# Kernel optimization log

Measured on AMD Instinct MI355X. Metric: run time of the kernel, lower is better.

Reference implementation:

```python
import jax, jax.numpy as jnp
import numpy as np

B, N = 8, 1024
C = [256, 512, 1024]
C2 = C[1]
KV = sum(C)            # 1792
H = 4                  # num_attention_heads
EXPAND = 4
LN_EPS = 1e-6
IN_EPS = 1e-5          # nn.InstanceNorm2d default eps


def setup_inputs() -> dict:
    key = jax.random.key(0)
    ks = jax.random.split(key, 16)
    s = 0.02
    inp = {
        "emb1": jax.random.normal(ks[0], (B, N, C[0]), jnp.float32),
        "emb2": jax.random.normal(ks[1], (B, N, C[1]), jnp.float32),
        "emb3": jax.random.normal(ks[2], (B, N, C[2]), jnp.float32),
        # per-head projection weights stored as [in, out] (torch Linear applies x @ W.T)
        "Wq": jax.random.normal(ks[3], (H, C2, C2), jnp.float32) * s,
        "Wk": jax.random.normal(ks[4], (H, KV, KV), jnp.float32) * s,
        "Wv": jax.random.normal(ks[5], (H, KV, KV), jnp.float32) * s,
        "Wout": jax.random.normal(ks[6], (C2, C2), jnp.float32) * s,
        "ln1_g": jnp.ones((C2,), jnp.float32),
        "ln1_b": jnp.zeros((C2,), jnp.float32),
        "lnall_g": jnp.ones((KV,), jnp.float32),
        "lnall_b": jnp.zeros((KV,), jnp.float32),
        "lnffn_g": jnp.ones((C2,), jnp.float32),
        "lnffn_b": jnp.zeros((C2,), jnp.float32),
        "fc1_w": jax.random.normal(ks[7], (C2, C2 * EXPAND), jnp.float32) * s,
        "fc1_b": jnp.zeros((C2 * EXPAND,), jnp.float32),
        "fc2_w": jax.random.normal(ks[8], (C2 * EXPAND, C2), jnp.float32) * s,
        "fc2_b": jnp.zeros((C2,), jnp.float32),
    }
    return inp


def _layer_norm(x, g, b, eps=LN_EPS):
    m = jnp.mean(x, axis=-1, keepdims=True)
    v = jnp.var(x, axis=-1, keepdims=True)
    return (x - m) * jax.lax.rsqrt(v + eps) * g + b


def _instance_norm2d(x, eps=IN_EPS):
    # x: [B, H, C2, KV]; normalize each (B,H) map over its last two dims (no affine)
    m = jnp.mean(x, axis=(-2, -1), keepdims=True)
    v = jnp.var(x, axis=(-2, -1), keepdims=True)
    return (x - m) * jax.lax.rsqrt(v + eps)


def reference(emb1, emb2, emb3, Wq, Wk, Wv, Wout,
              ln1_g, ln1_b, lnall_g, lnall_b, lnffn_g, lnffn_b,
              fc1_w, fc1_b, fc2_w, fc2_b):
    org2 = emb2
    emb_all = jnp.concatenate([emb1, emb2, emb3], axis=2)        # [B,N,KV]
    cx2 = _layer_norm(emb2, ln1_g, ln1_b)                         # [B,N,C2]
    emb_all = _layer_norm(emb_all, lnall_g, lnall_b)              # [B,N,KV]

    # batched per-head projections (replaces the Python ModuleList loop)
    q = jnp.einsum('bnc,hcd->bhnd', cx2, Wq)                      # [B,H,N,C2]
    k = jnp.einsum('bnc,hcd->bhnd', emb_all, Wk)                  # [B,H,N,KV]
    v = jnp.einsum('bnc,hcd->bhnd', emb_all, Wv)                  # [B,H,N,KV]

    # channel attention: q^T k over the token axis
    scores = jnp.einsum('bhnc,bhnk->bhck', q, k) / np.sqrt(KV)    # [B,H,C2,KV]
    probs = jax.nn.softmax(_instance_norm2d(scores), axis=3)      # [B,H,C2,KV]

    # context = probs @ v^T, then mean over heads (fused into one einsum)
    ctx = jnp.einsum('bhck,bhnk->bnc', probs, v) / H              # [B,N,C2]
    o = ctx @ Wout                                                # [B,N,C2]

    cx2 = org2 + o
    x2 = _layer_norm(cx2, lnffn_g, lnffn_b)
    x2 = jax.nn.gelu(x2 @ fc1_w + fc1_b, approximate=False)
    x2 = x2 @ fc2_w + fc2_b
    return x2 + cx2
```

## Files before the change

kernel.cpp:

```cpp
#include <hip/hip_runtime.h>
#include <cstdint>
#include <cmath>

typedef __bf16 bf16_t;
typedef __attribute__((ext_vector_type(8))) __bf16 bf16x8;
typedef __attribute__((ext_vector_type(4))) float f32x4;

#define AS_G(x) ((__attribute__((address_space(1))) void*)(x))
#define AS_L(x) ((__attribute__((address_space(3))) void*)(x))

#define BK 64

#define BSZ 8
#define NTOK 1024
#define CC2 512
#define KVD 1792
#define NH 4
#define FFD 2048
#define ROWS 8192


__device__ __forceinline__ void stage_pair(const bf16_t* __restrict__ A,
                                           const bf16_t* __restrict__ B,
                                           int ld, bf16_t* ldsA, bf16_t* ldsB, int tid)
{
#pragma unroll
  for (int it = 0; it < 4; ++it) {
    int chunk = it * 256 + tid;
    int r = chunk >> 3;
    int s = chunk & 7;
    int cg = ((s ^ (r & 7)) << 3);
    __builtin_amdgcn_global_load_lds(AS_G(A + (long)r * ld + cg),
                                     AS_L(ldsA + chunk * 8), 16, 0, 0);
    __builtin_amdgcn_global_load_lds(AS_G(B + (long)r * ld + cg),
                                     AS_L(ldsB + chunk * 8), 16, 0, 0);
  }
}

__device__ __forceinline__ void mfma_step(const bf16_t* ldsA, const bf16_t* ldsB,
                                          f32x4 acc[4][4], int wr, int wc, int lane, int kc)
{
  const int quad = lane >> 4, l16 = lane & 15;
  bf16x8 a[4], b[4];
#pragma unroll
  for (int i = 0; i < 4; ++i) {
    int r = wr * 64 + i * 16 + l16;
    int slot = (kc + quad) ^ (r & 7);
    a[i] = *(const bf16x8*)(ldsA + r * BK + slot * 8);
  }
#pragma unroll
  for (int j = 0; j < 4; ++j) {
    int r = wc * 64 + j * 16 + l16;
    int slot = (kc + quad) ^ (r & 7);
    b[j] = *(const bf16x8*)(ldsB + r * BK + slot * 8);
  }
#pragma unroll
  for (int i = 0; i < 4; ++i)
#pragma unroll
    for (int j = 0; j < 4; ++j)
      acc[i][j] = __builtin_amdgcn_mfma_f32_16x16x32_bf16(a[i], b[j], acc[i][j], 0, 0, 0);
}

#define GEMM_PROLOG() \
  __shared__ __align__(16) bf16_t ldsA[128 * BK]; \
  __shared__ __align__(16) bf16_t ldsB[128 * BK]; \
  const int tid = threadIdx.x; \
  const int wave = tid >> 6, lane = tid & 63; \
  const int wr = wave >> 1, wc = wave & 1; \
  f32x4 acc[4][4] = {};

#define GEMM_LOOP(Aptr, Bptr, Kdim) \
  for (int k0 = 0; k0 < (Kdim); k0 += BK) { \
    stage_pair((Aptr) + k0, (Bptr) + k0, (Kdim), ldsA, ldsB, tid); \
    __syncthreads(); \
    mfma_step(ldsA, ldsB, acc, wr, wc, lane, 0); \
    mfma_step(ldsA, ldsB, acc, wr, wc, lane, 4); \
    __syncthreads(); \
  }

template <typename F>
__device__ __forceinline__ void epilogue_apply(f32x4 acc[4][4], int wr, int wc, int lane, F f)
{
  const int quad = lane >> 4, l16 = lane & 15;
#pragma unroll
  for (int i = 0; i < 4; ++i)
#pragma unroll
    for (int j = 0; j < 4; ++j)
#pragma unroll
      for (int r = 0; r < 4; ++r)
        f(wr * 64 + i * 16 + quad * 4 + r, wc * 64 + j * 16 + l16, acc[i][j][r]);
}


__global__ void zstats_k(float* s)
{
  if (threadIdx.x < 64) s[threadIdx.x] = 0.f;
}

__global__ __launch_bounds__(256) void tconv_k(const float* __restrict__ in,
                                               bf16_t* __restrict__ out, int R, int Cc)
{
  __shared__ float tile[32][33];
  const long base = (long)blockIdx.z * R * Cc;
  const int c0 = blockIdx.x * 32, r0 = blockIdx.y * 32;
  const int tx = threadIdx.x & 31, ty = threadIdx.x >> 5;
#pragma unroll
  for (int i = 0; i < 4; ++i)
    tile[ty + i * 8][tx] = in[base + (long)(r0 + ty + i * 8) * Cc + c0 + tx];
  __syncthreads();
#pragma unroll
  for (int i = 0; i < 4; ++i)
    out[base + (long)(c0 + ty + i * 8) * R + r0 + tx] = (bf16_t)tile[tx][ty + i * 8];
}

__global__ __launch_bounds__(256) void tconv_bf_k(const bf16_t* __restrict__ in,
                                                  bf16_t* __restrict__ out, int R, int Cc)
{
  __shared__ float tile[32][33];
  const long base = (long)blockIdx.z * R * Cc;
  const int c0 = blockIdx.x * 32, r0 = blockIdx.y * 32;
  const int tx = threadIdx.x & 31, ty = threadIdx.x >> 5;
#pragma unroll
  for (int i = 0; i < 4; ++i)
    tile[ty + i * 8][tx] = (float)in[base + (long)(r0 + ty + i * 8) * Cc + c0 + tx];
  __syncthreads();
#pragma unroll
  for (int i = 0; i < 4; ++i)
    out[base + (long)(c0 + ty + i * 8) * R + r0 + tx] = (bf16_t)tile[tx][ty + i * 8];
}

__global__ __launch_bounds__(256) void cast_k(const float* __restrict__ in,
                                              bf16_t* __restrict__ out, long n)
{
  long i = ((long)blockIdx.x * 256 + threadIdx.x) * 4;
  if (i + 3 < n) {
    float4 v = *(const float4*)(in + i);
    out[i] = (bf16_t)v.x; out[i + 1] = (bf16_t)v.y;
    out[i + 2] = (bf16_t)v.z; out[i + 3] = (bf16_t)v.w;
  }
}

__global__ __launch_bounds__(256) void ln_concat_k(const float* __restrict__ e1,
                                                   const float* __restrict__ e2,
                                                   const float* __restrict__ e3,
                                                   const float* __restrict__ g1,
                                                   const float* __restrict__ b1,
                                                   const float* __restrict__ ga,
                                                   const float* __restrict__ ba,
                                                   bf16_t* __restrict__ cxln,
                                                   bf16_t* __restrict__ embln)
{
  const long row = blockIdx.x;
  const float* p1 = e1 + row * 256;
  const float* p2 = e2 + row * 512;
  const float* p3 = e3 + row * 1024;
  const int t = threadIdx.x;
  float vals[7];
  float sa = 0.f, qa = 0.f;
#pragma unroll
  for (int i = 0; i < 7; ++i) {
    int idx = t + i * 256;
    float x = (idx < 256) ? p1[idx] : (idx < 768 ? p2[idx - 256] : p3[idx - 768]);
    vals[i] = x;
    sa += x; qa += x * x;
  }
  float s2 = vals[1] + vals[2];
  float q2 = vals[1] * vals[1] + vals[2] * vals[2];
  for (int off = 32; off; off >>= 1) {
    sa += __shfl_down(sa, off, 64); qa += __shfl_down(qa, off, 64);
    s2 += __shfl_down(s2, off, 64); q2 += __shfl_down(q2, off, 64);
  }
  __shared__ float red[4][4];
  const int wave = t >> 6, lane = t & 63;
  if (lane == 0) { red[0][wave] = sa; red[1][wave] = qa; red[2][wave] = s2; red[3][wave] = q2; }
  __syncthreads();
  float SA = red[0][0] + red[0][1] + red[0][2] + red[0][3];
  float QA = red[1][0] + red[1][1] + red[1][2] + red[1][3];
  float S2 = red[2][0] + red[2][1] + red[2][2] + red[2][3];
  float Q2 = red[3][0] + red[3][1] + red[3][2] + red[3][3];
  float ma = SA * (1.f / 1792.f);
  float va = QA * (1.f / 1792.f) - ma * ma;
  float rsa = rsqrtf(va + 1e-6f);
  float m2 = S2 * (1.f / 512.f);
  float v2 = Q2 * (1.f / 512.f) - m2 * m2;
  float rs2 = rsqrtf(v2 + 1e-6f);
#pragma unroll
  for (int i = 0; i < 7; ++i) {
    int idx = t + i * 256;
    embln[row * 1792 + idx] = (bf16_t)((vals[i] - ma) * rsa * ga[idx] + ba[idx]);
  }
  cxln[row * 512 + t]       = (bf16_t)((vals[1] - m2) * rs2 * g1[t] + b1[t]);
  cxln[row * 512 + t + 256] = (bf16_t)((vals[2] - m2) * rs2 * g1[t + 256] + b1[t + 256]);
}

__global__ __launch_bounds__(256) void ln2_k(const float* __restrict__ X,
                                             const float* __restrict__ g,
                                             const float* __restrict__ bb,
                                             bf16_t* __restrict__ Y)
{
  const long row = blockIdx.x;
  const float* p = X + row * 512;
  const int t = threadIdx.x;
  float x0 = p[t], x1 = p[t + 256];
  float s = x0 + x1, q = x0 * x0 + x1 * x1;
  for (int off = 32; off; off >>= 1) {
    s += __shfl_down(s, off, 64); q += __shfl_down(q, off, 64);
  }
  __shared__ float red[2][4];
  const int wave = t >> 6, lane = t & 63;
  if (lane == 0) { red[0][wave] = s; red[1][wave] = q; }
  __syncthreads();
  float S = red[0][0] + red[0][1] + red[0][2] + red[0][3];
  float Q = red[1][0] + red[1][1] + red[1][2] + red[1][3];
  float m = S * (1.f / 512.f);
  float v = Q * (1.f / 512.f) - m * m;
  float rs = rsqrtf(v + 1e-6f);
  Y[row * 512 + t]       = (bf16_t)((x0 - m) * rs * g[t] + bb[t]);
  Y[row * 512 + t + 256] = (bf16_t)((x1 - m) * rs * g[t + 256] + bb[t + 256]);
}

__global__ __launch_bounds__(256) void softmax_k(bf16_t* __restrict__ SC,
                                                 const float* __restrict__ stats)
{
  const long rowid = blockIdx.x;
  const int z = (int)(rowid >> 9);
  const float inv_cnt = 1.f / (512.f * 1792.f);
  float m = stats[2 * z] * inv_cnt;
  float var = stats[2 * z + 1] * inv_cnt - m * m;
  float rs = rsqrtf(var + 1e-5f);
  bf16_t* rowp = SC + rowid * 1792;
  const int t = threadIdx.x;
  float v[7];
  float mx = -1e30f;
#pragma unroll
  for (int i = 0; i < 7; ++i) {
    v[i] = (float)rowp[t + i * 256] * rs;
    mx = fmaxf(mx, v[i]);
  }
  for (int off = 32; off; off >>= 1) mx = fmaxf(mx, __shfl_down(mx, off, 64));
  __shared__ float red[8];
  const int wave = t >> 6, lane = t & 63;
  if (lane == 0) red[wave] = mx;
  __syncthreads();
  mx = fmaxf(fmaxf(red[0], red[1]), fmaxf(red[2], red[3]));
  float sum = 0.f;
#pragma unroll
  for (int i = 0; i < 7; ++i) { v[i] = __expf(v[i] - mx); sum += v[i]; }
  for (int off = 32; off; off >>= 1) sum += __shfl_down(sum, off, 64);
  if (lane == 0) red[4 + wave] = sum;
  __syncthreads();
  float inv = 1.f / (red[4] + red[5] + red[6] + red[7]);
#pragma unroll
  for (int i = 0; i < 7; ++i) rowp[t + i * 256] = (bf16_t)(v[i] * inv);
}


__global__ __launch_bounds__(256) void gemm_ab(const bf16_t* __restrict__ A, long astride,
                                               const bf16_t* __restrict__ B, long bstride,
                                               bf16_t* __restrict__ C, long cstride,
                                               int K, int ldc)
{
  const int z = blockIdx.z;
  GEMM_PROLOG();
  const bf16_t* Ap = A + z * astride + (long)blockIdx.x * 128 * K;
  const bf16_t* Bp = B + z * bstride + (long)blockIdx.y * 128 * K;
  GEMM_LOOP(Ap, Bp, K);
  bf16_t* Cb = C + (long)z * cstride;
  const int rbase = blockIdx.x * 128, cbase = blockIdx.y * 128;
  epilogue_apply(acc, wr, wc, lane, [&](int rr, int cc, float v) {
    Cb[(long)(rbase + rr) * ldc + cbase + cc] = (bf16_t)v;
  });
}

__global__ __launch_bounds__(256) void gemm_t1(const bf16_t* __restrict__ WqT,
                                               const bf16_t* __restrict__ Gt,
                                               bf16_t* __restrict__ T1)
{
  const int z = blockIdx.z, hh = z >> 3, b = z & 7;
  GEMM_PROLOG();
  const bf16_t* Ap = WqT + (long)hh * CC2 * CC2 + (long)blockIdx.x * 128 * CC2;
  const bf16_t* Bp = Gt + (long)b * KVD * CC2 + (long)blockIdx.y * 128 * CC2;
  GEMM_LOOP(Ap, Bp, CC2);
  bf16_t* Cb = T1 + (long)z * CC2 * KVD;
  const int rbase = blockIdx.x * 128, cbase = blockIdx.y * 128;
  epilogue_apply(acc, wr, wc, lane, [&](int rr, int cc, float v) {
    Cb[(long)(rbase + rr) * KVD + cbase + cc] = (bf16_t)v;
  });
}

__global__ __launch_bounds__(256) void gemm_scores(const bf16_t* __restrict__ T1,
                                                   const bf16_t* __restrict__ WkT,
                                                   bf16_t* __restrict__ SC,
                                                   float* __restrict__ stats)
{
  const int z = blockIdx.z, hh = z >> 3;
  GEMM_PROLOG();
  const bf16_t* Ap = T1 + (long)z * CC2 * KVD + (long)blockIdx.x * 128 * KVD;
  const bf16_t* Bp = WkT + (long)hh * KVD * KVD + (long)blockIdx.y * 128 * KVD;
  GEMM_LOOP(Ap, Bp, KVD);
  const float scale = 0.02362277854f;
  bf16_t* Cb = SC + (long)z * CC2 * KVD;
  const int rbase = blockIdx.x * 128, cbase = blockIdx.y * 128;
  float s = 0.f, q = 0.f;
  epilogue_apply(acc, wr, wc, lane, [&](int rr, int cc, float v) {
    v *= scale;
    Cb[(long)(rbase + rr) * KVD + cbase + cc] = (bf16_t)v;
    s += v; q += v * v;
  });
  for (int off = 32; off; off >>= 1) { s += __shfl_down(s, off, 64); q += __shfl_down(q, off, 64); }
  __shared__ float red[8];
  if (lane == 0) { red[wave] = s; red[4 + wave] = q; }
  __syncthreads();
  if (tid == 0) {
    atomicAdd(&stats[2 * z],     red[0] + red[1] + red[2] + red[3]);
    atomicAdd(&stats[2 * z + 1], red[4] + red[5] + red[6] + red[7]);
  }
}

__global__ __launch_bounds__(256) void gemm_macc(const bf16_t* __restrict__ P,
                                                 const bf16_t* __restrict__ WvB,
                                                 bf16_t* __restrict__ M, int first)
{
  const int z = blockIdx.z, hh = z >> 3;
  GEMM_PROLOG();
  const bf16_t* Ap = P + (long)z * CC2 * KVD + (long)blockIdx.x * 128 * KVD;
  const bf16_t* Bp = WvB + (long)hh * KVD * KVD + (long)blockIdx.y * 128 * KVD;
  GEMM_LOOP(Ap, Bp, KVD);
  bf16_t* Cb = M + (long)z * CC2 * KVD;
  const int rbase = blockIdx.x * 128, cbase = blockIdx.y * 128;
  epilogue_apply(acc, wr, wc, lane, [&](int rr, int cc, float v) {
    long idx = (long)(rbase + rr) * KVD + cbase + cc;
    float prev = first ? 0.f : (float)Cb[idx];
    Cb[idx] = (bf16_t)(prev + v * 0.25f);
  });
}

__global__ __launch_bounds__(256) void gemm_ctx(const bf16_t* __restrict__ E,
                                                const bf16_t* __restrict__ Msum,
                                                bf16_t* __restrict__ CTX)
{
  const int b = blockIdx.z;
  GEMM_PROLOG();
  const bf16_t* Ap = E + (long)b * NTOK * KVD + (long)blockIdx.x * 128 * KVD;
  const bf16_t* Bp0 = Msum + (long)b * CC2 * KVD + (long)blockIdx.y * 128 * KVD;
  const bf16_t* Bp1 = Msum + (long)(8 + b) * CC2 * KVD + (long)blockIdx.y * 128 * KVD;
  GEMM_LOOP(Ap, Bp0, KVD);
  GEMM_LOOP(Ap, Bp1, KVD);
  bf16_t* Cb = CTX + (long)b * NTOK * CC2;
  const int rbase = blockIdx.x * 128, cbase = blockIdx.y * 128;
  epilogue_apply(acc, wr, wc, lane, [&](int rr, int cc, float v) {
    Cb[(long)(rbase + rr) * CC2 + cbase + cc] = (bf16_t)v;
  });
}

__global__ __launch_bounds__(256) void gemm_resid(const bf16_t* __restrict__ A,
                                                  const bf16_t* __restrict__ B,
                                                  const float* __restrict__ emb2,
                                                  float* __restrict__ CX2)
{
  GEMM_PROLOG();
  const bf16_t* Ap = A + (long)blockIdx.x * 128 * CC2;
  const bf16_t* Bp = B + (long)blockIdx.y * 128 * CC2;
  GEMM_LOOP(Ap, Bp, CC2);
  const int rbase = blockIdx.x * 128, cbase = blockIdx.y * 128;
  epilogue_apply(acc, wr, wc, lane, [&](int rr, int cc, float v) {
    long idx = (long)(rbase + rr) * CC2 + cbase + cc;
    CX2[idx] = v + emb2[idx];
  });
}

__global__ __launch_bounds__(256) void gemm_gelu(const bf16_t* __restrict__ A,
                                                 const bf16_t* __restrict__ B,
                                                 const float* __restrict__ bias,
                                                 bf16_t* __restrict__ H)
{
  GEMM_PROLOG();
  const bf16_t* Ap = A + (long)blockIdx.x * 128 * CC2;
  const bf16_t* Bp = B + (long)blockIdx.y * 128 * CC2;
  GEMM_LOOP(Ap, Bp, CC2);
  const int rbase = blockIdx.x * 128, cbase = blockIdx.y * 128;
  epilogue_apply(acc, wr, wc, lane, [&](int rr, int cc, float v) {
    float x = v + bias[cbase + cc];
    float g = 0.5f * x * (1.0f + erff(x * 0.70710678118f));
    H[(long)(rbase + rr) * FFD + cbase + cc] = (bf16_t)g;
  });
}

__global__ __launch_bounds__(256) void gemm_out(const bf16_t* __restrict__ A,
                                                const bf16_t* __restrict__ B,
                                                const float* __restrict__ bias,
                                                const float* __restrict__ CX2,
                                                float* __restrict__ OUT)
{
  GEMM_PROLOG();
  const bf16_t* Ap = A + (long)blockIdx.x * 128 * FFD;
  const bf16_t* Bp = B + (long)blockIdx.y * 128 * FFD;
  GEMM_LOOP(Ap, Bp, FFD);
  const int rbase = blockIdx.x * 128, cbase = blockIdx.y * 128;
  epilogue_apply(acc, wr, wc, lane, [&](int rr, int cc, float v) {
    long idx = (long)(rbase + rr) * CC2 + cbase + cc;
    OUT[idx] = v + bias[cbase + cc] + CX2[idx];
  });
}


extern "C" void kernel_launch(void* const* d_in, const int* in_sizes, int n_in,
                              void* d_out, int out_size, void* d_ws, size_t ws_size,
                              hipStream_t stream)
{
  const float* emb1   = (const float*)d_in[0];
  const float* emb2   = (const float*)d_in[1];
  const float* emb3   = (const float*)d_in[2];
  const float* Wq     = (const float*)d_in[3];
  const float* Wk     = (const float*)d_in[4];
  const float* Wv     = (const float*)d_in[5];
  const float* Wout   = (const float*)d_in[6];
  const float* ln1_g  = (const float*)d_in[7];
  const float* ln1_b  = (const float*)d_in[8];
  const float* lnall_g = (const float*)d_in[9];
  const float* lnall_b = (const float*)d_in[10];
  const float* lnffn_g = (const float*)d_in[11];
  const float* lnffn_b = (const float*)d_in[12];
  const float* fc1_w  = (const float*)d_in[13];
  const float* fc1_b  = (const float*)d_in[14];
  const float* fc2_w  = (const float*)d_in[15];
  const float* fc2_b  = (const float*)d_in[16];
  float* out = (float*)d_out;

  char* ws = (char*)d_ws;
  size_t off = 0;
  auto alloc = [&](size_t bytes) {
    size_t r = off;
    off = (off + bytes + 255) & ~(size_t)255;
    return r;
  };

  size_t oEMBLN = alloc((size_t)ROWS * KVD * 2);
  size_t oCXLN  = alloc((size_t)ROWS * CC2 * 2);
  size_t oCX2   = alloc((size_t)ROWS * CC2 * 4);
  size_t oGt    = alloc((size_t)BSZ * KVD * CC2 * 2);
  size_t oMsum  = alloc((size_t)16 * CC2 * KVD * 2);
  size_t oWOT   = alloc((size_t)CC2 * CC2 * 2);
  size_t oF1T   = alloc((size_t)FFD * CC2 * 2);
  size_t oF2T   = alloc((size_t)CC2 * FFD * 2);
  size_t oSTATS = alloc(64 * 4);
  size_t oSCR   = alloc(0);
  size_t oCXLNT  = alloc((size_t)BSZ * CC2 * NTOK * 2);
  size_t oEMBLNT = alloc((size_t)BSZ * KVD * NTOK * 2);
  (void)ws_size; (void)in_sizes; (void)n_in; (void)out_size;

  bf16_t* EMBLN  = (bf16_t*)(ws + oEMBLN);
  bf16_t* CXLN   = (bf16_t*)(ws + oCXLN);
  float*  CX2    = (float*)(ws + oCX2);
  bf16_t* Gt     = (bf16_t*)(ws + oGt);
  bf16_t* Msum   = (bf16_t*)(ws + oMsum);
  bf16_t* WOT    = (bf16_t*)(ws + oWOT);
  bf16_t* F1T    = (bf16_t*)(ws + oF1T);
  bf16_t* F2T    = (bf16_t*)(ws + oF2T);
  float*  STATS  = (float*)(ws + oSTATS);
  bf16_t* CXLNT  = (bf16_t*)(ws + oCXLNT);
  bf16_t* EMBLNT = (bf16_t*)(ws + oEMBLNT);
  char* scr = ws + oSCR;
  auto rnd = [](size_t v) { return (v + 255) & ~(size_t)255; };
  bf16_t* WqT = (bf16_t*)(scr);
  bf16_t* WkT = (bf16_t*)(scr + rnd((size_t)2 * CC2 * CC2 * 2));
  bf16_t* WvB = (bf16_t*)((char*)WkT + rnd((size_t)2 * KVD * KVD * 2));
  bf16_t* T1  = (bf16_t*)((char*)WvB + rnd((size_t)2 * KVD * KVD * 2));
  bf16_t* SC  = (bf16_t*)((char*)T1 + rnd((size_t)16 * CC2 * KVD * 2));
  bf16_t* CTX  = (bf16_t*)(scr);
  bf16_t* FFNH = (bf16_t*)(scr + rnd((size_t)ROWS * CC2 * 2));
  bf16_t* X2LN = CXLN;

  zstats_k<<<1, 64, 0, stream>>>(STATS);
  tconv_k<<<dim3(16, 16), 256, 0, stream>>>(Wout, WOT, 512, 512);
  tconv_k<<<dim3(64, 16), 256, 0, stream>>>(fc1_w, F1T, 512, 2048);
  tconv_k<<<dim3(16, 64), 256, 0, stream>>>(fc2_w, F2T, 2048, 512);

  ln_concat_k<<<8192, 256, 0, stream>>>(emb1, emb2, emb3, ln1_g, ln1_b,
                                        lnall_g, lnall_b, CXLN, EMBLN);

  tconv_bf_k<<<dim3(16, 32, 8), 256, 0, stream>>>(CXLN, CXLNT, 1024, 512);
  tconv_bf_k<<<dim3(56, 32, 8), 256, 0, stream>>>(EMBLN, EMBLNT, 1024, 1792);
  gemm_ab<<<dim3(14, 4, 8), 256, 0, stream>>>(EMBLNT, (long)KVD * NTOK,
                                              CXLNT, (long)CC2 * NTOK,
                                              Gt, (long)KVD * CC2, NTOK, CC2);

  for (int g = 0; g < 2; ++g) {
    tconv_k<<<dim3(16, 16, 2), 256, 0, stream>>>(Wq + (long)g * 2 * CC2 * CC2, WqT, 512, 512);
    tconv_k<<<dim3(56, 56, 2), 256, 0, stream>>>(Wk + (long)g * 2 * KVD * KVD, WkT, 1792, 1792);
    cast_k<<<6272, 256, 0, stream>>>(Wv + (long)g * 2 * KVD * KVD, WvB, (long)2 * KVD * KVD);

    gemm_t1<<<dim3(4, 14, 16), 256, 0, stream>>>(WqT, Gt, T1);
    gemm_scores<<<dim3(4, 14, 16), 256, 0, stream>>>(T1, WkT, SC, STATS + g * 32);
    softmax_k<<<8192, 256, 0, stream>>>(SC, STATS + g * 32);
    gemm_macc<<<dim3(4, 14, 16), 256, 0, stream>>>(SC, WvB, Msum, g == 0 ? 1 : 0);
  }

  gemm_ctx<<<dim3(8, 4, 8), 256, 0, stream>>>(EMBLN, Msum, CTX);

  gemm_resid<<<dim3(64, 4), 256, 0, stream>>>(CTX, WOT, emb2, CX2);

  ln2_k<<<8192, 256, 0, stream>>>(CX2, lnffn_g, lnffn_b, X2LN);
  gemm_gelu<<<dim3(64, 16), 256, 0, stream>>>(X2LN, F1T, fc1_b, FFNH);
  gemm_out<<<dim3(64, 4), 256, 0, stream>>>(FFNH, F2T, fc2_b, CX2, out);
}
```

Before: 913.6 us.

## Switch large batched GEMMs to 256x256 tiles with 8-wave ping-pong pipeline

Adds a 256x256-tile GEMM path with 512 threads, double-buffered LDS staging via direct global-to-LDS loads, XOR-swizzled LDS layout, and phased MFMA issue under s_setprio and barriers. It is applied to the T1, scores, macc and fc1-gelu GEMMs to raise arithmetic intensity and cut global traffic per FLOP. It also pre-adds the two head-group Msum partials in a small elementwise kernel so gemm_ctx runs one K loop instead of two. The cost is much larger LDS use (128KB per block) and more accumulator registers, which lowers occupancy. The 256-wide tiles also give fewer blocks for the smaller GEMMs.

Result: faster. 791.0 us (-13.4%).

```diff
diff --git a/kernel.cpp b/kernel.cpp
--- a/kernel.cpp
+++ b/kernel.cpp
@@ -92,6 +92,125 @@
 }
 
 
+__device__ __forceinline__ void stage256(const bf16_t* __restrict__ A,
+                                         const bf16_t* __restrict__ B,
+                                         int ld, bf16_t* ldsA, bf16_t* ldsB, int tid)
+{
+#pragma unroll
+  for (int it = 0; it < 4; ++it) {
+    int chunk = it * 512 + tid;
+    int r = chunk >> 3;
+    int s = chunk & 7;
+    int cg = ((s ^ (r & 7)) << 3);
+    __builtin_amdgcn_global_load_lds(AS_G(A + (long)r * ld + cg),
+                                     AS_L(ldsA + chunk * 8), 16, 0, 0);
+    __builtin_amdgcn_global_load_lds(AS_G(B + (long)r * ld + cg),
+                                     AS_L(ldsB + chunk * 8), 16, 0, 0);
+  }
+}
+
+__device__ __forceinline__ void qread_a(const bf16_t* ldsOp, int wr, int rh, int lane,
+                                        bf16x8 a[4][2])
+{
+  const int quad = lane >> 4, l16 = lane & 15;
+#pragma unroll
+  for (int mi = 0; mi < 4; ++mi)
+#pragma unroll
+    for (int kc = 0; kc < 2; ++kc) {
+      int r = wr * 128 + rh * 64 + mi * 16 + l16;
+      int slot = (kc * 4 + quad) ^ (r & 7);
+      a[mi][kc] = *(const bf16x8*)(ldsOp + r * BK + slot * 8);
+    }
+}
+
+__device__ __forceinline__ void qread_b(const bf16_t* ldsOp, int wc, int ch, int lane,
+                                        bf16x8 b[2][2])
+{
+  const int quad = lane >> 4, l16 = lane & 15;
+#pragma unroll
+  for (int nj = 0; nj < 2; ++nj)
+#pragma unroll
+    for (int kc = 0; kc < 2; ++kc) {
+      int r = wc * 64 + ch * 32 + nj * 16 + l16;
+      int slot = (kc * 4 + quad) ^ (r & 7);
+      b[nj][kc] = *(const bf16x8*)(ldsOp + r * BK + slot * 8);
+    }
+}
+
+template <int RH, int CH, bool TAIL>
+__device__ __forceinline__ void phase_mfma(f32x4 acc[8][4], const bf16x8 a[4][2],
+                                           const bf16x8 (&b)[2][2])
+{
+  if (!TAIL) {
+    __builtin_amdgcn_s_barrier();
+    asm volatile("s_waitcnt lgkmcnt(0)" ::: "memory");
+    __builtin_amdgcn_sched_barrier(0);
+  }
+  __builtin_amdgcn_s_setprio(1);
+#pragma unroll
+  for (int mi = 0; mi < 4; ++mi)
+#pragma unroll
+    for (int nj = 0; nj < 2; ++nj)
+#pragma unroll
+      for (int kc = 0; kc < 2; ++kc)
+        acc[RH * 4 + mi][CH * 2 + nj] =
+            __builtin_amdgcn_mfma_f32_16x16x32_bf16(a[mi][kc], b[nj][kc],
+                                                    acc[RH * 4 + mi][CH * 2 + nj], 0, 0, 0);
+  __builtin_amdgcn_s_setprio(0);
+  if (TAIL) __syncthreads();
+  else __builtin_amdgcn_s_barrier();
+}
+
+#define GEMM256_PROLOG() \
+  __shared__ __align__(16) bf16_t ldsA[2][256 * BK]; \
+  __shared__ __align__(16) bf16_t ldsB[2][256 * BK]; \
+  __shared__ float sred[16]; \
+  (void)sred; \
+  const int tid = threadIdx.x; \
+  const int wave = tid >> 6, lane = tid & 63; \
+  const int wr = wave >> 2, wc = wave & 3; \
+  f32x4 acc[8][4] = {};
+
+#define STAGE256(buf, t) stage256(Ap + (t) * BK, Bp + (t) * BK, Kd, ldsA[buf], ldsB[buf], tid)
+
+#define HALF_TILE(buf) \
+    qread_a(ldsA[buf], wr, 0, lane, a); \
+    qread_b(ldsB[buf], wc, 0, lane, b[0]); \
+    phase_mfma<0, 0, false>(acc, a, b[0]); \
+    qread_b(ldsB[buf], wc, 1, lane, b[1]); \
+    phase_mfma<0, 1, false>(acc, a, b[1]); \
+    qread_a(ldsA[buf], wr, 1, lane, a); \
+    phase_mfma<1, 0, false>(acc, a, b[0]); \
+    phase_mfma<1, 1, true>(acc, a, b[1]);
+
+#define GEMM256_LOOP(Aptr, Bptr, Kdim) { \
+  const bf16_t* Ap = (Aptr); const bf16_t* Bp = (Bptr); const int Kd = (Kdim); \
+  const int nit = Kd / (2 * BK); \
+  STAGE256(0, 0); \
+  __syncthreads(); \
+  for (int i = 0; i < nit; ++i) { \
+    bf16x8 a[4][2], b[2][2][2]; \
+    STAGE256(1, 2 * i + 1); \
+    HALF_TILE(0) \
+    if (i + 1 < nit) STAGE256(0, 2 * i + 2); \
+    HALF_TILE(1) \
+  } }
+
+template <typename F>
+__device__ __forceinline__ void epi256(f32x4 acc[8][4], int wr, int wc, int lane, F f)
+{
+  const int quad = lane >> 4, l16 = lane & 15;
+#pragma unroll
+  for (int i = 0; i < 8; ++i)
+#pragma unroll
+    for (int j = 0; j < 4; ++j)
+#pragma unroll
+      for (int r = 0; r < 4; ++r)
+        f(wr * 128 + (i >> 2) * 64 + (i & 3) * 16 + quad * 4 + r,
+          wc * 64 + (j >> 1) * 32 + (j & 1) * 16 + l16, acc[i][j][r]);
+}
+
+
 __global__ void zstats_k(float* s)
 {
   if (threadIdx.x < 64) s[threadIdx.x] = 0.f;
@@ -138,6 +257,18 @@
     out[i] = (bf16_t)v.x; out[i + 1] = (bf16_t)v.y;
     out[i + 2] = (bf16_t)v.z; out[i + 3] = (bf16_t)v.w;
   }
+}
+
+__global__ __launch_bounds__(256) void msum_add_k(const bf16_t* __restrict__ M,
+                                                  bf16_t* __restrict__ O)
+{
+  long i = ((long)blockIdx.x * 256 + threadIdx.x) * 8;
+  bf16x8 x = *(const bf16x8*)(M + i);
+  bf16x8 y = *(const bf16x8*)(M + (long)8 * CC2 * KVD + i);
+  bf16x8 r;
+#pragma unroll
+  for (int j = 0; j < 8; ++j) r[j] = (bf16_t)((float)x[j] + (float)y[j]);
+  *(bf16x8*)(O + i) = r;
 }
 
 __global__ __launch_bounds__(256) void ln_concat_k(const float* __restrict__ e1,
@@ -272,63 +403,65 @@
   });
 }
 
-__global__ __launch_bounds__(256) void gemm_t1(const bf16_t* __restrict__ WqT,
-                                               const bf16_t* __restrict__ Gt,
-                                               bf16_t* __restrict__ T1)
+__global__ __launch_bounds__(512, 2) void gemm_t1_256(const bf16_t* __restrict__ WqT,
+                                                      const bf16_t* __restrict__ Gt,
+                                                      bf16_t* __restrict__ T1)
 {
   const int z = blockIdx.z, hh = z >> 3, b = z & 7;
-  GEMM_PROLOG();
-  const bf16_t* Ap = WqT + (long)hh * CC2 * CC2 + (long)blockIdx.x * 128 * CC2;
-  const bf16_t* Bp = Gt + (long)b * KVD * CC2 + (long)blockIdx.y * 128 * CC2;
-  GEMM_LOOP(Ap, Bp, CC2);
+  GEMM256_PROLOG();
+  const bf16_t* Ap0 = WqT + (long)hh * CC2 * CC2 + (long)blockIdx.x * 256 * CC2;
+  const bf16_t* Bp0 = Gt + (long)b * KVD * CC2 + (long)blockIdx.y * 256 * CC2;
+  GEMM256_LOOP(Ap0, Bp0, CC2);
   bf16_t* Cb = T1 + (long)z * CC2 * KVD;
-  const int rbase = blockIdx.x * 128, cbase = blockIdx.y * 128;
-  epilogue_apply(acc, wr, wc, lane, [&](int rr, int cc, float v) {
+  const int rbase = blockIdx.x * 256, cbase = blockIdx.y * 256;
+  epi256(acc, wr, wc, lane, [&](int rr, int cc, float v) {
     Cb[(long)(rbase + rr) * KVD + cbase + cc] = (bf16_t)v;
   });
 }
 
-__global__ __launch_bounds__(256) void gemm_scores(const bf16_t* __restrict__ T1,
-                                                   const bf16_t* __restrict__ WkT,
-                                                   bf16_t* __restrict__ SC,
-                                                   float* __restrict__ stats)
+__global__ __launch_bounds__(512, 2) void gemm_scores_256(const bf16_t* __restrict__ T1,
+                                                          const bf16_t* __restrict__ WkT,
+                                                          bf16_t* __restrict__ SC,
+                                                          float* __restrict__ stats)
 {
   const int z = blockIdx.z, hh = z >> 3;
-  GEMM_PROLOG();
-  const bf16_t* Ap = T1 + (long)z * CC2 * KVD + (long)blockIdx.x * 128 * KVD;
-  const bf16_t* Bp = WkT + (long)hh * KVD * KVD + (long)blockIdx.y * 128 * KVD;
-  GEMM_LOOP(Ap, Bp, KVD);
+  GEMM256_PROLOG();
+  const bf16_t* Ap0 = T1 + (long)z * CC2 * KVD + (long)blockIdx.x * 256 * KVD;
+  const bf16_t* Bp0 = WkT + (long)hh * KVD * KVD + (long)blockIdx.y * 256 * KVD;
+  GEMM256_LOOP(Ap0, Bp0, KVD);
   const float scale = 0.02362277854f;
   bf16_t* Cb = SC + (long)z * CC2 * KVD;
-  const int rbase = blockIdx.x * 128, cbase = blockIdx.y * 128;
+  const int rbase = blockIdx.x * 256, cbase = blockIdx.y * 256;
   float s = 0.f, q = 0.f;
-  epilogue_apply(acc, wr, wc, lane, [&](int rr, int cc, float v) {
+  epi256(acc, wr, wc, lane, [&](int rr, int cc, float v) {
     v *= scale;
     Cb[(long)(rbase + rr) * KVD + cbase + cc] = (bf16_t)v;
     s += v; q += v * v;
   });
   for (int off = 32; off; off >>= 1) { s += __shfl_down(s, off, 64); q += __shfl_down(q, off, 64); }
-  __shared__ float red[8];
-  if (lane == 0) { red[wave] = s; red[4 + wave] = q; }
+  if (lane == 0) { sred[wave] = s; sred[8 + wave] = q; }
   __syncthreads();
   if (tid == 0) {
-    atomicAdd(&stats[2 * z],     red[0] + red[1] + red[2] + red[3]);
-    atomicAdd(&stats[2 * z + 1], red[4] + red[5] + red[6] + red[7]);
-  }
-}
-
-__global__ __launch_bounds__(256) void gemm_macc(const bf16_t* __restrict__ P,
-                                                 const bf16_t* __restrict__ WvB,
-                                                 bf16_t* __restrict__ M, int first)
+    float S = 0.f, Q = 0.f;
+#pragma unroll
+    for (int w = 0; w < 8; ++w) { S += sred[w]; Q += sred[8 + w]; }
+    atomicAdd(&stats[2 * z], S);
+    atomicAdd(&stats[2 * z + 1], Q);
+  }
+}
+
+__global__ __launch_bounds__(512, 2) void gemm_macc_256(const bf16_t* __restrict__ P,
+                                                        const bf16_t* __restrict__ WvB,
+                                                        bf16_t* __restrict__ M, int first)
 {
   const int z = blockIdx.z, hh = z >> 3;
-  GEMM_PROLOG();
-  const bf16_t* Ap = P + (long)z * CC2 * KVD + (long)blockIdx.x * 128 * KVD;
-  const bf16_t* Bp = WvB + (long)hh * KVD * KVD + (long)blockIdx.y * 128 * KVD;
-  GEMM_LOOP(Ap, Bp, KVD);
+  GEMM256_PROLOG();
+  const bf16_t* Ap0 = P + (long)z * CC2 * KVD + (long)blockIdx.x * 256 * KVD;
+  const bf16_t* Bp0 = WvB + (long)hh * KVD * KVD + (long)blockIdx.y * 256 * KVD;
+  GEMM256_LOOP(Ap0, Bp0, KVD);
   bf16_t* Cb = M + (long)z * CC2 * KVD;
-  const int rbase = blockIdx.x * 128, cbase = blockIdx.y * 128;
-  epilogue_apply(acc, wr, wc, lane, [&](int rr, int cc, float v) {
+  const int rbase = blockIdx.x * 256, cbase = blockIdx.y * 256;
+  epi256(acc, wr, wc, lane, [&](int rr, int cc, float v) {
     long idx = (long)(rbase + rr) * KVD + cbase + cc;
     float prev = first ? 0.f : (float)Cb[idx];
     Cb[idx] = (bf16_t)(prev + v * 0.25f);
@@ -336,16 +469,14 @@
 }
 
 __global__ __launch_bounds__(256) void gemm_ctx(const bf16_t* __restrict__ E,
-                                                const bf16_t* __restrict__ Msum,
+                                                const bf16_t* __restrict__ Msum8,
                                                 bf16_t* __restrict__ CTX)
 {
   const int b = blockIdx.z;
   GEMM_PROLOG();
   const bf16_t* Ap = E + (long)b * NTOK * KVD + (long)blockIdx.x * 128 * KVD;
-  const bf16_t* Bp0 = Msum + (long)b * CC2 * KVD + (long)blockIdx.y * 128 * KVD;
-  const bf16_t* Bp1 = Msum + (long)(8 + b) * CC2 * KVD + (long)blockIdx.y * 128 * KVD;
-  GEMM_LOOP(Ap, Bp0, KVD);
-  GEMM_LOOP(Ap, Bp1, KVD);
+  const bf16_t* Bp = Msum8 + (long)b * CC2 * KVD + (long)blockIdx.y * 128 * KVD;
+  GEMM_LOOP(Ap, Bp, KVD);
   bf16_t* Cb = CTX + (long)b * NTOK * CC2;
   const int rbase = blockIdx.x * 128, cbase = blockIdx.y * 128;
   epilogue_apply(acc, wr, wc, lane, [&](int rr, int cc, float v) {
@@ -369,17 +500,17 @@
   });
 }
 
-__global__ __launch_bounds__(256) void gemm_gelu(const bf16_t* __restrict__ A,
-                                                 const bf16_t* __restrict__ B,
-                                                 const float* __restrict__ bias,
-                                                 bf16_t* __restrict__ H)
-{
-  GEMM_PROLOG();
-  const bf16_t* Ap = A + (long)blockIdx.x * 128 * CC2;
-  const bf16_t* Bp = B + (long)blockIdx.y * 128 * CC2;
-  GEMM_LOOP(Ap, Bp, CC2);
-  const int rbase = blockIdx.x * 128, cbase = blockIdx.y * 128;
-  epilogue_apply(acc, wr, wc, lane, [&](int rr, int cc, float v) {
+__global__ __launch_bounds__(512, 2) void gemm_gelu_256(const bf16_t* __restrict__ A,
+                                                        const bf16_t* __restrict__ B,
+                                                        const float* __restrict__ bias,
+                                                        bf16_t* __restrict__ H)
+{
+  GEMM256_PROLOG();
+  const bf16_t* Ap0 = A + (long)blockIdx.x * 256 * CC2;
+  const bf16_t* Bp0 = B + (long)blockIdx.y * 256 * CC2;
+  GEMM256_LOOP(Ap0, Bp0, CC2);
+  const int rbase = blockIdx.x * 256, cbase = blockIdx.y * 256;
+  epi256(acc, wr, wc, lane, [&](int rr, int cc, float v) {
     float x = v + bias[cbase + cc];
     float g = 0.5f * x * (1.0f + erff(x * 0.70710678118f));
     H[(long)(rbase + rr) * FFD + cbase + cc] = (bf16_t)g;
@@ -467,8 +598,9 @@
   bf16_t* WvB = (bf16_t*)((char*)WkT + rnd((size_t)2 * KVD * KVD * 2));
   bf16_t* T1  = (bf16_t*)((char*)WvB + rnd((size_t)2 * KVD * KVD * 2));
   bf16_t* SC  = (bf16_t*)((char*)T1 + rnd((size_t)16 * CC2 * KVD * 2));
-  bf16_t* CTX  = (bf16_t*)(scr);
-  bf16_t* FFNH = (bf16_t*)(scr + rnd((size_t)ROWS * CC2 * 2));
+  bf16_t* Msum8 = (bf16_t*)(scr);
+  bf16_t* CTX   = (bf16_t*)(scr + rnd((size_t)8 * CC2 * KVD * 2));
+  bf16_t* FFNH  = (bf16_t*)((char*)CTX + rnd((size_t)ROWS * CC2 * 2));
   bf16_t* X2LN = CXLN;
 
   zstats_k<<<1, 64, 0, stream>>>(STATS);
@@ -490,17 +622,18 @@
     tconv_k<<<dim3(56, 56, 2), 256, 0, stream>>>(Wk + (long)g * 2 * KVD * KVD, WkT, 1792, 1792);
     cast_k<<<6272, 256, 0, stream>>>(Wv + (long)g * 2 * KVD * KVD, WvB, (long)2 * KVD * KVD);
 
-    gemm_t1<<<dim3(4, 14, 16), 256, 0, stream>>>(WqT, Gt, T1);
-    gemm_scores<<<dim3(4, 14, 16), 256, 0, stream>>>(T1, WkT, SC, STATS + g * 32);
+    gemm_t1_256<<<dim3(2, 7, 16), 512, 0, stream>>>(WqT, Gt, T1);
+    gemm_scores_256<<<dim3(2, 7, 16), 512, 0, stream>>>(T1, WkT, SC, STATS + g * 32);
     softmax_k<<<8192, 256, 0, stream>>>(SC, STATS + g * 32);
-    gemm_macc<<<dim3(4, 14, 16), 256, 0, stream>>>(SC, WvB, Msum, g == 0 ? 1 : 0);
-  }
-
-  gemm_ctx<<<dim3(8, 4, 8), 256, 0, stream>>>(EMBLN, Msum, CTX);
+    gemm_macc_256<<<dim3(2, 7, 16), 512, 0, stream>>>(SC, WvB, Msum, g == 0 ? 1 : 0);
+  }
+
+  msum_add_k<<<3584, 256, 0, stream>>>(Msum, Msum8);
+  gemm_ctx<<<dim3(8, 4, 8), 256, 0, stream>>>(EMBLN, Msum8, CTX);
 
   gemm_resid<<<dim3(64, 4), 256, 0, stream>>>(CTX, WOT, emb2, CX2);
 
   ln2_k<<<8192, 256, 0, stream>>>(CX2, lnffn_g, lnffn_b, X2LN);
-  gemm_gelu<<<dim3(64, 16), 256, 0, stream>>>(X2LN, F1T, fc1_b, FFNH);
+  gemm_gelu_256<<<dim3(32, 8), 512, 0, stream>>>(X2LN, F1T, fc1_b, FFNH);
   gemm_out<<<dim3(64, 4), 256, 0, stream>>>(FFNH, F2T, fc2_b, CX2, out);
 }
```
